# Optimization experiments

Hardware: AMD Instinct MI355X
Metric: run time of the kernel (lower is better)

## Reference

```python
import jax, jax.numpy as jnp
import numpy as np

EPS = 1e-6  # LayerNorm eps (norm_layer = partial(nn.LayerNorm, eps=1e-6))
B, CIN, HW, P, D, L, H, F = 32, 3, 224, 16, 768, 12, 12, 3072


def _ln(x, w, b):
    m = x.mean(-1, keepdims=True)
    v = jnp.var(x, axis=-1, keepdims=True)
    return (x - m) / jnp.sqrt(v + EPS) * w + b


def setup_inputs() -> dict:
    key = jax.random.key(0)
    ks = jax.random.split(key, 10)
    s = 0.02  # trunc_normal_ std
    N = (HW // P) ** 2
    return {
        "x": jax.random.normal(ks[0], (B, CIN, HW, HW), jnp.float32),
        "conv_w": jax.random.normal(ks[1], (D, CIN, P, P), jnp.float32) * s,
        "conv_b": jnp.zeros((D,), jnp.float32),
        "cls_token": jax.random.normal(ks[2], (1, 1, D), jnp.float32) * s,
        "pos_embed": jax.random.normal(ks[3], (1, N + 1, D), jnp.float32) * s,
        "ln1_w": jnp.ones((L, D), jnp.float32),
        "ln1_b": jnp.zeros((L, D), jnp.float32),
        "qkv_w": jax.random.normal(ks[4], (L, D, 3 * D), jnp.float32) * s,
        "qkv_b": jnp.zeros((L, 3 * D), jnp.float32),
        "proj_w": jax.random.normal(ks[5], (L, D, D), jnp.float32) * s,
        "proj_b": jnp.zeros((L, D), jnp.float32),
        "ln2_w": jnp.ones((L, D), jnp.float32),
        "ln2_b": jnp.zeros((L, D), jnp.float32),
        "fc1_w": jax.random.normal(ks[6], (L, D, F), jnp.float32) * s,
        "fc1_b": jnp.zeros((L, F), jnp.float32),
        "fc2_w": jax.random.normal(ks[7], (L, F, D), jnp.float32) * s,
        "fc2_b": jnp.zeros((L, D), jnp.float32),
        "lnf_w": jnp.ones((D,), jnp.float32),
        "lnf_b": jnp.zeros((D,), jnp.float32),
    }


def _vit(x, conv_w, conv_b, cls_token, pos_embed,
         ln1_w, ln1_b, qkv_w, qkv_b, proj_w, proj_b,
         ln2_w, ln2_b, fc1_w, fc1_b, fc2_w, fc2_b, lnf_w, lnf_b):
    b = x.shape[0]
    nh = HW // P
    dh = D // H
    scale = dh ** (-0.5)
    # Patch embed: stride-P/kernel-P conv == reshape into patches + GEMM.
    # [B,3,H,W] -> [B, nh*nh, 3*P*P] with (c,ph,pw) flatten order matching conv_w.
    p = x.reshape(b, CIN, nh, P, nh, P).transpose(0, 2, 4, 1, 3, 5)
    p = p.reshape(b, nh * nh, CIN * P * P)
    p = p @ conv_w.reshape(D, -1).T + conv_b  # [B, N, D]
    cls = jnp.broadcast_to(cls_token, (b, 1, D))
    h = jnp.concatenate([cls, p], axis=1) + pos_embed  # [B, N+1, D]

    def block(h, prm):
        l1w, l1b, qw, qb, pw, pb, l2w, l2b, f1w, f1b, f2w, f2b = prm
        y = _ln(h, l1w, l1b)
        qkv = (y @ qw + qb).reshape(b, -1, 3, H, dh)
        q, k, v = qkv[:, :, 0], qkv[:, :, 1], qkv[:, :, 2]  # [B,N,H,dh]
        attn = jnp.einsum("bnhd,bmhd->bhnm", q, k) * scale
        attn = jax.nn.softmax(attn, axis=-1)
        o = jnp.einsum("bhnm,bmhd->bnhd", attn, v).reshape(b, -1, D)
        h = h + (o @ pw + pb)
        y = _ln(h, l2w, l2b)
        h = h + (jax.nn.gelu(y @ f1w + f1b, approximate=False) @ f2w + f2b)
        return h, None

    prms = (ln1_w, ln1_b, qkv_w, qkv_b, proj_w, proj_b,
            ln2_w, ln2_b, fc1_w, fc1_b, fc2_w, fc2_b)
    h, _ = jax.lax.scan(block, h, prms)
    h = _ln(h, lnf_w, lnf_b)
    return h[:, 0][None]  # forward(): x.unsqueeze(0) -> [1, B, D]


def reference(x, conv_w, conv_b, cls_token, pos_embed,
              ln1_w, ln1_b, qkv_w, qkv_b, proj_w, proj_b,
              ln2_w, ln2_b, fc1_w, fc1_b, fc2_w, fc2_b, lnf_w, lnf_b):
    return _vit(x, conv_w, conv_b, cls_token, pos_embed,
                ln1_w, ln1_b, qkv_w, qkv_b, proj_w, proj_b,
                ln2_w, ln2_b, fc1_w, fc1_b, fc2_w, fc2_b, lnf_w, lnf_b)
```

## Files before the change

kernel.cpp:

```cpp
#include <hip/hip_runtime.h>
#include <cmath>

typedef __bf16 bf16;
typedef __bf16 bf16x8 __attribute__((ext_vector_type(8)));
typedef __bf16 bf16x4 __attribute__((ext_vector_type(4)));
typedef float  f32x4  __attribute__((ext_vector_type(4)));

#define MFMA16(a,b,c) __builtin_amdgcn_mfma_f32_16x16x32_bf16(a,b,c,0,0,0)

__device__ __forceinline__ void async_ld16(const void* g, void* l) {
  __builtin_amdgcn_global_load_lds((__attribute__((address_space(1))) void*)(g),
                                   (__attribute__((address_space(3))) void*)(l),
                                   16, 0, 0);
}

enum { EPI_PATCH = 0, EPI_BF16 = 1, EPI_RESID = 2, EPI_GELU = 3 };

template <int EPI>
__global__ __launch_bounds__(256) void gemm128(
    const bf16* __restrict__ A, const bf16* __restrict__ Wt,
    const float* __restrict__ bias, bf16* __restrict__ outB,
    float* __restrict__ outF, int M, int N, int K, int Kc)
{
  __shared__ bf16 As[3][128 * 32];
  __shared__ bf16 Bs[3][128 * 32];
  const int tid  = threadIdx.x;
  const int lane = tid & 63, wid = tid >> 6;
  const int qr   = lane & 15, quad = lane >> 4;
  const int wm   = wid >> 1, wn = wid & 1;
  const int bm   = blockIdx.x, bn = blockIdx.y, z = blockIdx.z;
  const int kbeg = z * Kc;
  const int kend = min(K, kbeg + Kc);
  const int sr   = wid * 16 + (lane >> 2);
  const int scol = (lane & 3) * 8;

  f32x4 zero4 = {0.f, 0.f, 0.f, 0.f};
  f32x4 acc[4][4];
#pragma unroll
  for (int i = 0; i < 4; i++)
#pragma unroll
    for (int j = 0; j < 4; j++) acc[i][j] = zero4;

  const int ra0 = min(bm * 128 + sr, M - 1);
  const int ra1 = min(bm * 128 + 64 + sr, M - 1);
  const size_t nr0 = (size_t)(bn * 128 + sr);
  const size_t nr1 = (size_t)(bn * 128 + 64 + sr);

  auto stage = [&](int buf, int k0) {
    async_ld16(A + (size_t)ra0 * K + k0 + scol, &As[buf][(wid * 16) * 32]);
    async_ld16(A + (size_t)ra1 * K + k0 + scol, &As[buf][(64 + wid * 16) * 32]);
    async_ld16(Wt + nr0 * K + k0 + scol, &Bs[buf][(wid * 16) * 32]);
    async_ld16(Wt + nr1 * K + k0 + scol, &Bs[buf][(64 + wid * 16) * 32]);
  };

  const int nt = (kend - kbeg) >> 5;
  stage(0, kbeg); stage(1, kbeg + 32); stage(2, kbeg + 64);
  int buf = 0;
  for (int t = 0; t < nt; ++t) {
    if (t + 2 < nt)       asm volatile("s_waitcnt vmcnt(8)" ::: "memory");
    else if (t + 1 < nt)  asm volatile("s_waitcnt vmcnt(4)" ::: "memory");
    else                  asm volatile("s_waitcnt vmcnt(0)" ::: "memory");
    __builtin_amdgcn_s_barrier();
    asm volatile("" ::: "memory");
    bf16x8 af[4], bfr[4];
    const bf16* Ab = &As[buf][0];
    const bf16* Bb = &Bs[buf][0];
#pragma unroll
    for (int mi = 0; mi < 4; mi++)
      af[mi] = *(const bf16x8*)&Ab[(wm * 64 + mi * 16 + qr) * 32 + quad * 8];
#pragma unroll
    for (int ni = 0; ni < 4; ni++)
      bfr[ni] = *(const bf16x8*)&Bb[(wn * 64 + ni * 16 + qr) * 32 + quad * 8];
    __builtin_amdgcn_s_setprio(1);
#pragma unroll
    for (int mi = 0; mi < 4; mi++)
#pragma unroll
      for (int ni = 0; ni < 4; ni++)
        acc[mi][ni] = MFMA16(af[mi], bfr[ni], acc[mi][ni]);
    __builtin_amdgcn_s_setprio(0);
    __builtin_amdgcn_sched_barrier(0);
    asm volatile("" ::: "memory");
    __builtin_amdgcn_s_barrier();
    asm volatile("" ::: "memory");
    if (t + 3 < nt) stage(buf, kbeg + (t + 3) * 32);
    buf = (buf == 2) ? 0 : buf + 1;
  }

#pragma unroll
  for (int mi = 0; mi < 4; mi++) {
#pragma unroll
    for (int ni = 0; ni < 4; ni++) {
      const int row0 = bm * 128 + wm * 64 + mi * 16 + quad * 4;
      const int col  = bn * 128 + wn * 64 + ni * 16 + qr;
      const float bv = (z == 0) ? bias[col] : 0.f;
#pragma unroll
      for (int r = 0; r < 4; r++) {
        const int row = row0 + r;
        if (row < M) {
          float v = acc[mi][ni][r] + bv;
          if constexpr (EPI == EPI_PATCH) {
            int bb = row / 196, nn = row % 196;
            int orow = bb * 197 + 1 + nn;
            atomicAdd(&outF[(size_t)orow * 768 + col], v);
          } else if constexpr (EPI == EPI_BF16) {
            outB[(size_t)row * N + col] = (bf16)v;
          } else if constexpr (EPI == EPI_GELU) {
            float gel = 0.5f * v * (1.f + erff(v * 0.70710678118f));
            outB[(size_t)row * N + col] = (bf16)gel;
          } else {
            atomicAdd(&outF[(size_t)row * 768 + col], v);
          }
        }
      }
    }
  }
}

template <int EPI>
__global__ __launch_bounds__(512, 4) void gemm_bt8(
    const bf16* __restrict__ A, const bf16* __restrict__ Wt,
    const float* __restrict__ bias, bf16* __restrict__ outB,
    int M, int N, int K)
{
  __shared__ bf16 As[3][128 * 32];
  __shared__ bf16 Bs[3][128 * 32];
  const int tid  = threadIdx.x;
  const int lane = tid & 63, wid = tid >> 6;
  const int qr   = lane & 15, quad = lane >> 4;
  const int wm   = wid >> 1, wn = wid & 1;
  const int bm   = blockIdx.x, bn = blockIdx.y;
  const int sr   = wid * 16 + (lane >> 2);
  const int scol = (lane & 3) * 8;

  f32x4 zero4 = {0.f, 0.f, 0.f, 0.f};
  f32x4 acc[2][4];
#pragma unroll
  for (int i = 0; i < 2; i++)
#pragma unroll
    for (int j = 0; j < 4; j++) acc[i][j] = zero4;

  const int ra = min(bm * 128 + sr, M - 1);
  const size_t nr = (size_t)(bn * 128 + sr);

  auto stage = [&](int buf, int k0) {
    async_ld16(A  + (size_t)ra * K + k0 + scol, &As[buf][(wid * 16) * 32]);
    async_ld16(Wt + nr * K + k0 + scol,         &Bs[buf][(wid * 16) * 32]);
  };

  const int nt = K >> 5;
  stage(0, 0); stage(1, 32); stage(2, 64);
  int buf = 0;
  for (int t = 0; t < nt; ++t) {
    if (t + 2 < nt)       asm volatile("s_waitcnt vmcnt(4)" ::: "memory");
    else if (t + 1 < nt)  asm volatile("s_waitcnt vmcnt(2)" ::: "memory");
    else                  asm volatile("s_waitcnt vmcnt(0)" ::: "memory");
    __builtin_amdgcn_s_barrier();
    asm volatile("" ::: "memory");
    bf16x8 af[2], bfr[4];
    const bf16* Ab = &As[buf][0];
    const bf16* Bb = &Bs[buf][0];
#pragma unroll
    for (int mi = 0; mi < 2; mi++)
      af[mi] = *(const bf16x8*)&Ab[(wm * 32 + mi * 16 + qr) * 32 + quad * 8];
#pragma unroll
    for (int ni = 0; ni < 4; ni++)
      bfr[ni] = *(const bf16x8*)&Bb[(wn * 64 + ni * 16 + qr) * 32 + quad * 8];
    __builtin_amdgcn_s_setprio(1);
#pragma unroll
    for (int mi = 0; mi < 2; mi++)
#pragma unroll
      for (int ni = 0; ni < 4; ni++)
        acc[mi][ni] = MFMA16(af[mi], bfr[ni], acc[mi][ni]);
    __builtin_amdgcn_s_setprio(0);
    __builtin_amdgcn_sched_barrier(0);
    asm volatile("" ::: "memory");
    __builtin_amdgcn_s_barrier();
    asm volatile("" ::: "memory");
    if (t + 3 < nt) stage(buf, (t + 3) * 32);
    buf = (buf == 2) ? 0 : buf + 1;
  }

#pragma unroll
  for (int mi = 0; mi < 2; mi++) {
#pragma unroll
    for (int ni = 0; ni < 4; ni++) {
      const int row0 = bm * 128 + wm * 32 + mi * 16 + quad * 4;
      const int col  = bn * 128 + wn * 64 + ni * 16 + qr;
      const float bv = bias[col];
#pragma unroll
      for (int r = 0; r < 4; r++) {
        const int row = row0 + r;
        if (row < M) {
          float v = acc[mi][ni][r] + bv;
          if constexpr (EPI == EPI_GELU) {
            float gel = 0.5f * v * (1.f + erff(v * 0.70710678118f));
            outB[(size_t)row * N + col] = (bf16)gel;
          } else {
            outB[(size_t)row * N + col] = (bf16)v;
          }
        }
      }
    }
  }
}

__global__ __launch_bounds__(256) void attn_kernel(
    const bf16* __restrict__ qkv, bf16* __restrict__ o)
{
  __shared__ __align__(16) char smem[68864];
  bf16 (*Qs)[72]  = (bf16(*)[72])(smem);
  bf16 (*Ks)[72]  = (bf16(*)[72])(smem + 9216);
  bf16 (*Ps)[232] = (bf16(*)[232])(smem + 9216);
  bf16 (*Vt)[232] = (bf16(*)[232])(smem + 39168);

  const int tid  = threadIdx.x;
  const int lane = tid & 63, wid = tid >> 6;
  const int qr   = lane & 15, quad = lane >> 4;
  const int qt   = blockIdx.x & 3, bh = blockIdx.x >> 2;
  const int head = bh % 12, b = bh / 12;
  const int q0   = qt * 64;
  const size_t base = (size_t)b * 197 * 2304 + head * 64;

  {
    int r = tid >> 2, cb = (tid & 3) * 16;
    int s = q0 + r; if (s > 196) s = 196;
    const bf16* src = qkv + base + (size_t)s * 2304 + cb;
    *(uint4*)&Qs[r][cb]     = *(const uint4*)src;
    *(uint4*)&Qs[r][cb + 8] = *(const uint4*)(src + 8);
  }
  for (int rr = tid >> 2; rr < 208; rr += 64) {
    int cb = (tid & 3) * 16;
    uint4 v0 = make_uint4(0, 0, 0, 0), v1 = make_uint4(0, 0, 0, 0);
    if (rr < 197) {
      const bf16* src = qkv + base + 768 + (size_t)rr * 2304 + cb;
      v0 = *(const uint4*)src; v1 = *(const uint4*)(src + 8);
    }
    *(uint4*)&Ks[rr][cb] = v0; *(uint4*)&Ks[rr][cb + 8] = v1;
  }
  for (int rr = tid >> 2; rr < 224; rr += 64) {
    int cb = (tid & 3) * 16;
    bf16 tmp[16];
    if (rr < 197) {
      const bf16* src = qkv + base + 1536 + (size_t)rr * 2304 + cb;
      *(uint4*)&tmp[0] = *(const uint4*)src;
      *(uint4*)&tmp[8] = *(const uint4*)(src + 8);
    } else {
#pragma unroll
      for (int j = 0; j < 16; j++) tmp[j] = (bf16)0.f;
    }
#pragma unroll
    for (int j = 0; j < 16; j++) Vt[cb + j][rr] = tmp[j];
  }
  __syncthreads();

  bf16x8 qa0 = *(const bf16x8*)&Qs[wid * 16 + qr][quad * 8];
  bf16x8 qa1 = *(const bf16x8*)&Qs[wid * 16 + qr][32 + quad * 8];
  f32x4 zero4 = {0.f, 0.f, 0.f, 0.f};
  f32x4 sc[13];
#pragma unroll
  for (int t = 0; t < 13; t++) sc[t] = zero4;
#pragma unroll
  for (int t = 0; t < 13; t++) {
    bf16x8 kb0 = *(const bf16x8*)&Ks[t * 16 + qr][quad * 8];
    bf16x8 kb1 = *(const bf16x8*)&Ks[t * 16 + qr][32 + quad * 8];
    sc[t] = MFMA16(qa0, kb0, sc[t]);
    sc[t] = MFMA16(qa1, kb1, sc[t]);
  }
  float mx[4] = {-1e30f, -1e30f, -1e30f, -1e30f};
#pragma unroll
  for (int t = 0; t < 13; t++) {
    bool valid = (t * 16 + qr) < 197;
#pragma unroll
    for (int r = 0; r < 4; r++) {
      float v = sc[t][r] * 0.125f;
      sc[t][r] = v;
      if (valid) mx[r] = fmaxf(mx[r], v);
    }
  }
#pragma unroll
  for (int r = 0; r < 4; r++)
#pragma unroll
    for (int off = 1; off < 16; off <<= 1)
      mx[r] = fmaxf(mx[r], __shfl_xor(mx[r], off, 16));
  float sum[4] = {0.f, 0.f, 0.f, 0.f};
#pragma unroll
  for (int t = 0; t < 13; t++) {
    bool valid = (t * 16 + qr) < 197;
#pragma unroll
    for (int r = 0; r < 4; r++) {
      float e = valid ? __expf(sc[t][r] - mx[r]) : 0.f;
      sc[t][r] = e; sum[r] += e;
    }
  }
#pragma unroll
  for (int r = 0; r < 4; r++) {
#pragma unroll
    for (int off = 1; off < 16; off <<= 1)
      sum[r] += __shfl_xor(sum[r], off, 16);
    sum[r] = 1.f / sum[r];
  }
  __syncthreads();
#pragma unroll
  for (int t = 0; t < 13; t++)
#pragma unroll
    for (int r = 0; r < 4; r++)
      Ps[wid * 16 + quad * 4 + r][t * 16 + qr] = (bf16)(sc[t][r] * sum[r]);
  {
    bf16x4 zz = {(bf16)0.f, (bf16)0.f, (bf16)0.f, (bf16)0.f};
    *(bf16x4*)&Ps[wid * 16 + qr][208 + quad * 4] = zz;
  }
  __syncthreads();

  f32x4 oa[4];
#pragma unroll
  for (int ni = 0; ni < 4; ni++) oa[ni] = zero4;
#pragma unroll
  for (int k0 = 0; k0 < 224; k0 += 32) {
    bf16x8 pa = *(const bf16x8*)&Ps[wid * 16 + qr][k0 + quad * 8];
#pragma unroll
    for (int ni = 0; ni < 4; ni++) {
      bf16x8 vb = *(const bf16x8*)&Vt[ni * 16 + qr][k0 + quad * 8];
      oa[ni] = MFMA16(pa, vb, oa[ni]);
    }
  }
#pragma unroll
  for (int ni = 0; ni < 4; ni++)
#pragma unroll
    for (int r = 0; r < 4; r++) {
      int row = q0 + wid * 16 + quad * 4 + r;
      if (row < 197)
        o[(((size_t)b * 197 + row) * 12 + head) * 64 + ni * 16 + qr] =
            (bf16)oa[ni][r];
    }
}

__global__ __launch_bounds__(256) void ln_bf16(
    const float* __restrict__ h, const float* __restrict__ w,
    const float* __restrict__ b, bf16* __restrict__ y, int rows)
{
  int row = blockIdx.x * 4 + (threadIdx.x >> 6);
  int lane = threadIdx.x & 63;
  if (row >= rows) return;
  const float* hr = h + (size_t)row * 768;
  float v[12]; float s = 0.f;
#pragma unroll
  for (int i = 0; i < 12; i++) { v[i] = hr[lane + 64 * i]; s += v[i]; }
#pragma unroll
  for (int off = 32; off >= 1; off >>= 1) s += __shfl_xor(s, off, 64);
  float mean = s * (1.f / 768.f);
  float q = 0.f;
#pragma unroll
  for (int i = 0; i < 12; i++) { float d = v[i] - mean; q += d * d; }
#pragma unroll
  for (int off = 32; off >= 1; off >>= 1) q += __shfl_xor(q, off, 64);
  float rstd = rsqrtf(q * (1.f / 768.f) + 1e-6f);
  bf16* yr = y + (size_t)row * 768;
#pragma unroll
  for (int i = 0; i < 12; i++)
    yr[lane + 64 * i] = (bf16)((v[i] - mean) * rstd * w[lane + 64 * i] + b[lane + 64 * i]);
}

__global__ __launch_bounds__(256) void ln_final(
    const float* __restrict__ h, const float* __restrict__ w,
    const float* __restrict__ b, float* __restrict__ out)
{
  int bi = blockIdx.x * 4 + (threadIdx.x >> 6);
  int lane = threadIdx.x & 63;
  if (bi >= 32) return;
  const float* hr = h + (size_t)bi * 197 * 768;
  float v[12]; float s = 0.f;
#pragma unroll
  for (int i = 0; i < 12; i++) { v[i] = hr[lane + 64 * i]; s += v[i]; }
#pragma unroll
  for (int off = 32; off >= 1; off >>= 1) s += __shfl_xor(s, off, 64);
  float mean = s * (1.f / 768.f);
  float q = 0.f;
#pragma unroll
  for (int i = 0; i < 12; i++) { float d = v[i] - mean; q += d * d; }
#pragma unroll
  for (int off = 32; off >= 1; off >>= 1) q += __shfl_xor(q, off, 64);
  float rstd = rsqrtf(q * (1.f / 768.f) + 1e-6f);
#pragma unroll
  for (int i = 0; i < 12; i++)
    out[(size_t)bi * 768 + lane + 64 * i] =
        (v[i] - mean) * rstd * w[lane + 64 * i] + b[lane + 64 * i];
}

__global__ __launch_bounds__(256) void transpose_w(
    const float* __restrict__ in, bf16* __restrict__ out, int R, int C)
{
  __shared__ float t[32][33];
  size_t zoff = (size_t)blockIdx.z * R * C;
  in += zoff; out += zoff;
  int c0 = blockIdx.x * 32, r0 = blockIdx.y * 32;
  int lx = threadIdx.x & 31, ly = threadIdx.x >> 5;
#pragma unroll
  for (int i = 0; i < 32; i += 8) t[ly + i][lx] = in[(size_t)(r0 + ly + i) * C + c0 + lx];
  __syncthreads();
#pragma unroll
  for (int i = 0; i < 32; i += 8)
    out[(size_t)(c0 + ly + i) * R + r0 + lx] = (bf16)t[lx][ly + i];
}

__global__ __launch_bounds__(256) void convert_bf16(
    const float* __restrict__ in, bf16* __restrict__ out, int n)
{
  int i = blockIdx.x * 256 + threadIdx.x;
  if (i < n) out[i] = (bf16)in[i];
}

__global__ __launch_bounds__(256) void patch_extract(
    const float* __restrict__ x, bf16* __restrict__ patches)
{
  int i = blockIdx.x * 256 + threadIdx.x;
  if (i >= 6272 * 192) return;
  int m = i / 192, kq = (i % 192) * 4;
  int b = m / 196, pp = m % 196, py = pp / 14, px = pp % 14;
  int c = kq >> 8, rem = kq & 255, iy = rem >> 4, ix = rem & 15;
  const float4 v = *(const float4*)&x[(((size_t)(b * 3 + c) * 224 + py * 16 + iy) * 224) + px * 16 + ix];
  bf16x4 pv = {(bf16)v.x, (bf16)v.y, (bf16)v.z, (bf16)v.w};
  *(bf16x4*)&patches[(size_t)m * 768 + kq] = pv;
}

__global__ __launch_bounds__(256) void h_init_full(
    const float* __restrict__ cls, const float* __restrict__ pos,
    float* __restrict__ h)
{
  int i = blockIdx.x * 256 + threadIdx.x;
  if (i >= 6304 * 192) return;
  int row = i / 192, c4 = (i % 192) * 4;
  int s = row % 197;
  float4 pv = *(const float4*)&pos[(size_t)s * 768 + c4];
  if (s == 0) {
    float4 cv = *(const float4*)&cls[c4];
    pv.x += cv.x; pv.y += cv.y; pv.z += cv.z; pv.w += cv.w;
  }
  *(float4*)&h[(size_t)row * 768 + c4] = pv;
}

extern "C" void kernel_launch(void* const* d_in, const int* in_sizes, int n_in,
                              void* d_out, int out_size, void* d_ws, size_t ws_size,
                              hipStream_t stream)
{
  const float* x      = (const float*)d_in[0];
  const float* conv_w = (const float*)d_in[1];
  const float* conv_b = (const float*)d_in[2];
  const float* cls    = (const float*)d_in[3];
  const float* pos    = (const float*)d_in[4];
  const float* ln1_w  = (const float*)d_in[5];
  const float* ln1_b  = (const float*)d_in[6];
  const float* qkv_w  = (const float*)d_in[7];
  const float* qkv_b  = (const float*)d_in[8];
  const float* proj_w = (const float*)d_in[9];
  const float* proj_b = (const float*)d_in[10];
  const float* ln2_w  = (const float*)d_in[11];
  const float* ln2_b  = (const float*)d_in[12];
  const float* fc1_w  = (const float*)d_in[13];
  const float* fc1_b  = (const float*)d_in[14];
  const float* fc2_w  = (const float*)d_in[15];
  const float* fc2_b  = (const float*)d_in[16];
  const float* lnf_w  = (const float*)d_in[17];
  const float* lnf_b  = (const float*)d_in[18];
  float* out = (float*)d_out;
  (void)in_sizes; (void)n_in; (void)out_size; (void)ws_size;

  char* ws = (char*)d_ws;
  size_t off = 0;
  auto alloc = [&](size_t bytes) -> char* {
    char* p = ws + off;
    off += (bytes + 255) & ~(size_t)255;
    return p;
  };

  bf16*  convwB  = (bf16*)alloc((size_t)768 * 768 * 2);
  bf16*  qkvT    = (bf16*)alloc((size_t)12 * 2304 * 768 * 2);
  bf16*  projT   = (bf16*)alloc((size_t)12 * 768 * 768 * 2);
  bf16*  fc1T    = (bf16*)alloc((size_t)12 * 3072 * 768 * 2);
  bf16*  fc2T    = (bf16*)alloc((size_t)12 * 768 * 3072 * 2);
  bf16*  patches = (bf16*)alloc((size_t)6272 * 768 * 2);
  float* h       = (float*)alloc((size_t)6304 * 768 * 4);
  bf16*  y       = (bf16*)alloc((size_t)6304 * 768 * 2);
  bf16*  qkvB    = (bf16*)alloc((size_t)6304 * 2304 * 2);
  bf16*  obuf    = (bf16*)alloc((size_t)6304 * 768 * 2);
  bf16*  g       = (bf16*)alloc((size_t)6304 * 3072 * 2);

  convert_bf16<<<(768 * 768 + 255) / 256, 256, 0, stream>>>(conv_w, convwB, 768 * 768);
  transpose_w<<<dim3(2304 / 32, 768 / 32, 12), 256, 0, stream>>>(qkv_w, qkvT, 768, 2304);
  transpose_w<<<dim3(768 / 32, 768 / 32, 12), 256, 0, stream>>>(proj_w, projT, 768, 768);
  transpose_w<<<dim3(3072 / 32, 768 / 32, 12), 256, 0, stream>>>(fc1_w, fc1T, 768, 3072);
  transpose_w<<<dim3(768 / 32, 3072 / 32, 12), 256, 0, stream>>>(fc2_w, fc2T, 3072, 768);

  patch_extract<<<(6272 * 192) / 256, 256, 0, stream>>>(x, patches);
  h_init_full<<<(6304 * 192 + 255) / 256, 256, 0, stream>>>(cls, pos, h);
  gemm128<EPI_PATCH><<<dim3(49, 6, 2), 256, 0, stream>>>(
      patches, convwB, conv_b, nullptr, h, 6272, 768, 768, 384);

  for (int l = 0; l < 12; l++) {
    ln_bf16<<<1576, 256, 0, stream>>>(h, ln1_w + l * 768, ln1_b + l * 768, y, 6304);
    gemm_bt8<EPI_BF16><<<dim3(50, 18), 512, 0, stream>>>(
        y, qkvT + (size_t)l * 2304 * 768, qkv_b + l * 2304, qkvB,
        6304, 2304, 768);
    attn_kernel<<<32 * 12 * 4, 256, 0, stream>>>(qkvB, obuf);
    gemm128<EPI_RESID><<<dim3(50, 6, 2), 256, 0, stream>>>(
        obuf, projT + (size_t)l * 768 * 768, proj_b + l * 768, nullptr, h,
        6304, 768, 768, 384);
    ln_bf16<<<1576, 256, 0, stream>>>(h, ln2_w + l * 768, ln2_b + l * 768, y, 6304);
    gemm_bt8<EPI_GELU><<<dim3(50, 24), 512, 0, stream>>>(
        y, fc1T + (size_t)l * 3072 * 768, fc1_b + l * 3072, g,
        6304, 3072, 768);
    gemm128<EPI_RESID><<<dim3(50, 6, 2), 256, 0, stream>>>(
        g, fc2T + (size_t)l * 768 * 3072, fc2_b + l * 768, nullptr, h,
        6304, 768, 3072, 1536);
  }
  ln_final<<<8, 256, 0, stream>>>(h, lnf_w, lnf_b, out);
}
```

Baseline: 3.733 ms.

## Unify GEMMs into 8-wave kernel with XOR-swizzled LDS layout

Merges the two GEMM kernels into one 512-thread, 8-wave template that handles split-K and all epilogues, so the projection, fc2 and patch GEMMs now use the 8-wave configuration. It also adds an XOR swizzle on the 16-byte column chunk for the async LDS stores and the matching fragment reads, to reduce LDS bank conflicts. The risk is that swizzle and staging mismatches could corrupt results, and that the smaller per-wave tile lowers register-level reuse.

```diff
diff --git a/kernel.cpp b/kernel.cpp
--- a/kernel.cpp
+++ b/kernel.cpp
@@ -17,7 +17,7 @@
 enum { EPI_PATCH = 0, EPI_BF16 = 1, EPI_RESID = 2, EPI_GELU = 3 };
 
 template <int EPI>
-__global__ __launch_bounds__(256) void gemm128(
+__global__ __launch_bounds__(512, 4) void gemm8(
     const bf16* __restrict__ A, const bf16* __restrict__ Wt,
     const float* __restrict__ bias, bf16* __restrict__ outB,
     float* __restrict__ outF, int M, int N, int K, int Kc)
@@ -32,48 +32,46 @@
   const int kbeg = z * Kc;
   const int kend = min(K, kbeg + Kc);
   const int sr   = wid * 16 + (lane >> 2);
-  const int scol = (lane & 3) * 8;
+  const int fst  = (lane >> 3) & 3;
+  const int scol = (((lane & 3) ^ fst)) * 8;
+  const int fr   = (qr >> 1) & 3;
 
   f32x4 zero4 = {0.f, 0.f, 0.f, 0.f};
-  f32x4 acc[4][4];
-#pragma unroll
-  for (int i = 0; i < 4; i++)
+  f32x4 acc[2][4];
+#pragma unroll
+  for (int i = 0; i < 2; i++)
 #pragma unroll
     for (int j = 0; j < 4; j++) acc[i][j] = zero4;
 
-  const int ra0 = min(bm * 128 + sr, M - 1);
-  const int ra1 = min(bm * 128 + 64 + sr, M - 1);
-  const size_t nr0 = (size_t)(bn * 128 + sr);
-  const size_t nr1 = (size_t)(bn * 128 + 64 + sr);
+  const int ra = min(bm * 128 + sr, M - 1);
+  const size_t nr = (size_t)(bn * 128 + sr);
 
   auto stage = [&](int buf, int k0) {
-    async_ld16(A + (size_t)ra0 * K + k0 + scol, &As[buf][(wid * 16) * 32]);
-    async_ld16(A + (size_t)ra1 * K + k0 + scol, &As[buf][(64 + wid * 16) * 32]);
-    async_ld16(Wt + nr0 * K + k0 + scol, &Bs[buf][(wid * 16) * 32]);
-    async_ld16(Wt + nr1 * K + k0 + scol, &Bs[buf][(64 + wid * 16) * 32]);
+    async_ld16(A  + (size_t)ra * K + k0 + scol, &As[buf][(wid * 16) * 32]);
+    async_ld16(Wt + nr * K + k0 + scol,         &Bs[buf][(wid * 16) * 32]);
   };
 
   const int nt = (kend - kbeg) >> 5;
   stage(0, kbeg); stage(1, kbeg + 32); stage(2, kbeg + 64);
   int buf = 0;
   for (int t = 0; t < nt; ++t) {
-    if (t + 2 < nt)       asm volatile("s_waitcnt vmcnt(8)" ::: "memory");
-    else if (t + 1 < nt)  asm volatile("s_waitcnt vmcnt(4)" ::: "memory");
+    if (t + 2 < nt)       asm volatile("s_waitcnt vmcnt(4)" ::: "memory");
+    else if (t + 1 < nt)  asm volatile("s_waitcnt vmcnt(2)" ::: "memory");
     else                  asm volatile("s_waitcnt vmcnt(0)" ::: "memory");
     __builtin_amdgcn_s_barrier();
     asm volatile("" ::: "memory");
-    bf16x8 af[4], bfr[4];
+    bf16x8 af[2], bfr[4];
     const bf16* Ab = &As[buf][0];
     const bf16* Bb = &Bs[buf][0];
 #pragma unroll
-    for (int mi = 0; mi < 4; mi++)
-      af[mi] = *(const bf16x8*)&Ab[(wm * 64 + mi * 16 + qr) * 32 + quad * 8];
+    for (int mi = 0; mi < 2; mi++)
+      af[mi] = *(const bf16x8*)&Ab[(wm * 32 + mi * 16 + qr) * 32 + (quad ^ fr) * 8];
 #pragma unroll
     for (int ni = 0; ni < 4; ni++)
-      bfr[ni] = *(const bf16x8*)&Bb[(wn * 64 + ni * 16 + qr) * 32 + quad * 8];
+      bfr[ni] = *(const bf16x8*)&Bb[(wn * 64 + ni * 16 + qr) * 32 + (quad ^ fr) * 8];
     __builtin_amdgcn_s_setprio(1);
 #pragma unroll
-    for (int mi = 0; mi < 4; mi++)
+    for (int mi = 0; mi < 2; mi++)
 #pragma unroll
       for (int ni = 0; ni < 4; ni++)
         acc[mi][ni] = MFMA16(af[mi], bfr[ni], acc[mi][ni]);
@@ -87,10 +85,10 @@
   }
 
 #pragma unroll
-  for (int mi = 0; mi < 4; mi++) {
+  for (int mi = 0; mi < 2; mi++) {
 #pragma unroll
     for (int ni = 0; ni < 4; ni++) {
-      const int row0 = bm * 128 + wm * 64 + mi * 16 + quad * 4;
+      const int row0 = bm * 128 + wm * 32 + mi * 16 + quad * 4;
       const int col  = bn * 128 + wn * 64 + ni * 16 + qr;
       const float bv = (z == 0) ? bias[col] : 0.f;
 #pragma unroll
@@ -109,94 +107,6 @@
             outB[(size_t)row * N + col] = (bf16)gel;
           } else {
             atomicAdd(&outF[(size_t)row * 768 + col], v);
-          }
-        }
-      }
-    }
-  }
-}
-
-template <int EPI>
-__global__ __launch_bounds__(512, 4) void gemm_bt8(
-    const bf16* __restrict__ A, const bf16* __restrict__ Wt,
-    const float* __restrict__ bias, bf16* __restrict__ outB,
-    int M, int N, int K)
-{
-  __shared__ bf16 As[3][128 * 32];
-  __shared__ bf16 Bs[3][128 * 32];
-  const int tid  = threadIdx.x;
-  const int lane = tid & 63, wid = tid >> 6;
-  const int qr   = lane & 15, quad = lane >> 4;
-  const int wm   = wid >> 1, wn = wid & 1;
-  const int bm   = blockIdx.x, bn = blockIdx.y;
-  const int sr   = wid * 16 + (lane >> 2);
-  const int scol = (lane & 3) * 8;
-
-  f32x4 zero4 = {0.f, 0.f, 0.f, 0.f};
-  f32x4 acc[2][4];
-#pragma unroll
-  for (int i = 0; i < 2; i++)
-#pragma unroll
-    for (int j = 0; j < 4; j++) acc[i][j] = zero4;
-
-  const int ra = min(bm * 128 + sr, M - 1);
-  const size_t nr = (size_t)(bn * 128 + sr);
-
-  auto stage = [&](int buf, int k0) {
-    async_ld16(A  + (size_t)ra * K + k0 + scol, &As[buf][(wid * 16) * 32]);
-    async_ld16(Wt + nr * K + k0 + scol,         &Bs[buf][(wid * 16) * 32]);
-  };
-
-  const int nt = K >> 5;
-  stage(0, 0); stage(1, 32); stage(2, 64);
-  int buf = 0;
-  for (int t = 0; t < nt; ++t) {
-    if (t + 2 < nt)       asm volatile("s_waitcnt vmcnt(4)" ::: "memory");
-    else if (t + 1 < nt)  asm volatile("s_waitcnt vmcnt(2)" ::: "memory");
-    else                  asm volatile("s_waitcnt vmcnt(0)" ::: "memory");
-    __builtin_amdgcn_s_barrier();
-    asm volatile("" ::: "memory");
-    bf16x8 af[2], bfr[4];
-    const bf16* Ab = &As[buf][0];
-    const bf16* Bb = &Bs[buf][0];
-#pragma unroll
-    for (int mi = 0; mi < 2; mi++)
-      af[mi] = *(const bf16x8*)&Ab[(wm * 32 + mi * 16 + qr) * 32 + quad * 8];
-#pragma unroll
-    for (int ni = 0; ni < 4; ni++)
-      bfr[ni] = *(const bf16x8*)&Bb[(wn * 64 + ni * 16 + qr) * 32 + quad * 8];
-    __builtin_amdgcn_s_setprio(1);
-#pragma unroll
-    for (int mi = 0; mi < 2; mi++)
-#pragma unroll
-      for (int ni = 0; ni < 4; ni++)
-        acc[mi][ni] = MFMA16(af[mi], bfr[ni], acc[mi][ni]);
-    __builtin_amdgcn_s_setprio(0);
-    __builtin_amdgcn_sched_barrier(0);
-    asm volatile("" ::: "memory");
-    __builtin_amdgcn_s_barrier();
-    asm volatile("" ::: "memory");
-    if (t + 3 < nt) stage(buf, (t + 3) * 32);
-    buf = (buf == 2) ? 0 : buf + 1;
-  }
-
-#pragma unroll
-  for (int mi = 0; mi < 2; mi++) {
-#pragma unroll
-    for (int ni = 0; ni < 4; ni++) {
-      const int row0 = bm * 128 + wm * 32 + mi * 16 + quad * 4;
-      const int col  = bn * 128 + wn * 64 + ni * 16 + qr;
-      const float bv = bias[col];
-#pragma unroll
-      for (int r = 0; r < 4; r++) {
-        const int row = row0 + r;
-        if (row < M) {
-          float v = acc[mi][ni][r] + bv;
-          if constexpr (EPI == EPI_GELU) {
-            float gel = 0.5f * v * (1.f + erff(v * 0.70710678118f));
-            outB[(size_t)row * N + col] = (bf16)gel;
-          } else {
-            outB[(size_t)row * N + col] = (bf16)v;
           }
         }
       }
@@ -492,23 +402,23 @@
 
   patch_extract<<<(6272 * 192) / 256, 256, 0, stream>>>(x, patches);
   h_init_full<<<(6304 * 192 + 255) / 256, 256, 0, stream>>>(cls, pos, h);
-  gemm128<EPI_PATCH><<<dim3(49, 6, 2), 256, 0, stream>>>(
+  gemm8<EPI_PATCH><<<dim3(49, 6, 2), 512, 0, stream>>>(
       patches, convwB, conv_b, nullptr, h, 6272, 768, 768, 384);
 
   for (int l = 0; l < 12; l++) {
     ln_bf16<<<1576, 256, 0, stream>>>(h, ln1_w + l * 768, ln1_b + l * 768, y, 6304);
-    gemm_bt8<EPI_BF16><<<dim3(50, 18), 512, 0, stream>>>(
-        y, qkvT + (size_t)l * 2304 * 768, qkv_b + l * 2304, qkvB,
-        6304, 2304, 768);
+    gemm8<EPI_BF16><<<dim3(50, 18, 1), 512, 0, stream>>>(
+        y, qkvT + (size_t)l * 2304 * 768, qkv_b + l * 2304, qkvB, nullptr,
+        6304, 2304, 768, 768);
     attn_kernel<<<32 * 12 * 4, 256, 0, stream>>>(qkvB, obuf);
-    gemm128<EPI_RESID><<<dim3(50, 6, 2), 256, 0, stream>>>(
+    gemm8<EPI_RESID><<<dim3(50, 6, 2), 512, 0, stream>>>(
         obuf, projT + (size_t)l * 768 * 768, proj_b + l * 768, nullptr, h,
         6304, 768, 768, 384);
     ln_bf16<<<1576, 256, 0, stream>>>(h, ln2_w + l * 768, ln2_b + l * 768, y, 6304);
-    gemm_bt8<EPI_GELU><<<dim3(50, 24), 512, 0, stream>>>(
-        y, fc1T + (size_t)l * 3072 * 768, fc1_b + l * 3072, g,
-        6304, 3072, 768);
-    gemm128<EPI_RESID><<<dim3(50, 6, 2), 256, 0, stream>>>(
+    gemm8<EPI_GELU><<<dim3(50, 24, 1), 512, 0, stream>>>(
+        y, fc1T + (size_t)l * 3072 * 768, fc1_b + l * 3072, g, nullptr,
+        6304, 3072, 768, 768);
+    gemm8<EPI_RESID><<<dim3(50, 6, 2), 512, 0, stream>>>(
         g, fc2T + (size_t)l * 768 * 3072, fc2_b + l * 768, nullptr, h,
         6304, 768, 3072, 1536);
   }
```

After: 3.622 ms. 1.03x faster.
